# Kernel tuning notes

Hardware: AMD Instinct MI355X
Metric: run time of the kernel (lower is better)

## Reference

```python
import jax, jax.numpy as jnp
import numpy as np

# TT config: input_dimension=2048, output_multiplier=4, rank=16
# top_ranks    = [8,2,2,2,2,2,2,2,2]  (prod = 2048)
# bottom_ranks = [8,2,2,2,2,2,2,2,2]  (prod = 2048)
# core shapes (top, bottom, left, right): left/right are TT bond ranks.
CORE_SHAPES = [(8, 8, 1, 16)] + [(2, 2, 16, 16)] * 7 + [(2, 2, 16, 1)]


def setup_inputs() -> dict:
    key = jax.random.key(0)
    ks = jax.random.split(key, 10)
    inp = {"x": jax.random.normal(ks[0], (4, 2048, 2048), dtype=jnp.float32)}
    for i, s in enumerate(CORE_SHAPES):
        inp[f"p{i}"] = jax.random.normal(ks[i + 1], s, dtype=jnp.float32)
    return inp


def _tt_apply(x, ps):
    # x: [B, S, D] with D = prod(top_ranks) = 2048
    B, S, D = x.shape
    T = B * S
    # Normalize every core to (top, bottom, left_bond_in, right_bond_out).
    # Original einsum: '... abcdefghi, ajs, bkst, cltu, dmuv, envw, fowx, gpxy, hqzy, irz -> ... jklmnopqr'
    # Core 7 ('hqzy') has swapped bonds: its 4th dim (y) is the incoming bond
    # from core 6 and its 3rd dim (z) is the outgoing bond into core 8 ('irz').
    cores = list(ps[:7]) + [jnp.transpose(ps[7], (0, 1, 3, 2)), ps[8]]
    # core 0 is used as p0[:, :, 0, :] in the original; its left dim is 1 so
    # keeping the singleton left axis is identical math.
    y = x.reshape(T, 1, 1, D)  # [T, out_so_far=1, bond=1, remaining_top=D]
    J, M = 1, D
    for g in cores:
        tk, bk, lk, rk = g.shape
        y = y.reshape(T, J, lk, tk, M // tk)
        # contract incoming bond l and current top index a with the core
        y = jnp.einsum('tjlam,ablr->tjbrm', y, g)
        J *= bk
        M //= tk
        y = y.reshape(T, J, rk, M)
    # final: rk == 1, M == 1 -> [T, J] with J = prod(bottom_ranks) = 2048
    return y.reshape(B, S, J)


def reference(x, p0, p1, p2, p3, p4, p5, p6, p7, p8):
    return _tt_apply(x, (p0, p1, p2, p3, p4, p5, p6, p7, p8))
```

## Files before the change

kernel.cpp:

```cpp
#include <hip/hip_runtime.h>
#include <stdint.h>

typedef unsigned short u16;
typedef __bf16 bf16x8 __attribute__((ext_vector_type(8)));
typedef float f32x16 __attribute__((ext_vector_type(16)));
typedef u16 u16x8 __attribute__((ext_vector_type(8)));

__device__ __forceinline__ u16 f2bf(float f) {
  uint32_t u = __float_as_uint(f);
  u += 0x7fffu + ((u >> 16) & 1u);
  return (u16)(u >> 16);
}

__global__ __launch_bounds__(256) void build_lr_kernel(
    const float* __restrict__ p0, const float* __restrict__ p1,
    const float* __restrict__ p2, const float* __restrict__ p3,
    const float* __restrict__ p4, const float* __restrict__ p5,
    const float* __restrict__ p6, const float* __restrict__ p7,
    const float* __restrict__ p8, float* __restrict__ L4, float* __restrict__ R) {
  __shared__ float sC[5 * 1024];
  const int tid = threadIdx.x;
  if (blockIdx.x < 64) {
    for (int i = tid; i < 1024; i += 256) {
      sC[i]        = p0[i];
      sC[1024 + i] = p1[i];
      sC[2048 + i] = p2[i];
      sC[3072 + i] = p3[i];
      sC[4096 + i] = p4[i];
    }
    __syncthreads();
    const int idx = blockIdx.x * 256 + tid;
    const int AL = idx >> 7, BL = idx & 127;
    float t[16], u[16];
    const float* c0 = sC + ((AL >> 4) * 8 + (BL >> 4)) * 16;
#pragma unroll
    for (int l = 0; l < 16; l++) t[l] = c0[l];
#pragma unroll
    for (int k = 0; k < 4; k++) {
      const int ak = (AL >> (3 - k)) & 1;
      const int bk = (BL >> (3 - k)) & 1;
      const float* ck = sC + (k + 1) * 1024 + ((ak * 2 + bk) << 8);
#pragma unroll
      for (int r = 0; r < 16; r++) u[r] = 0.f;
#pragma unroll
      for (int l = 0; l < 16; l++) {
        const float tv = t[l];
#pragma unroll
        for (int r = 0; r < 16; r++) u[r] += tv * ck[l * 16 + r];
      }
#pragma unroll
      for (int r = 0; r < 16; r++) t[r] = u[r];
    }
    float4* dst = (float4*)(L4 + (size_t)idx * 16);
#pragma unroll
    for (int j = 0; j < 4; j++)
      dst[j] = make_float4(t[4 * j], t[4 * j + 1], t[4 * j + 2], t[4 * j + 3]);
  } else {
    for (int i = tid; i < 1024; i += 256) {
      sC[i]        = p5[i];
      sC[1024 + i] = p6[i];
      sC[2048 + i] = p7[i];
    }
    for (int i = tid; i < 64; i += 256) sC[3072 + i] = p8[i];
    __syncthreads();
    const int AR = tid >> 4, BR = tid & 15;
    const int a5 = AR >> 3, a6 = (AR >> 2) & 1, a7 = (AR >> 1) & 1, a8 = AR & 1;
    const int b5 = BR >> 3, b6 = (BR >> 2) & 1, b7 = (BR >> 1) & 1, b8 = BR & 1;
    float t[16], u[16];
    const float* c8 = sC + 3072 + (a8 * 2 + b8) * 16;
#pragma unroll
    for (int l = 0; l < 16; l++) t[l] = c8[l];
    const float* c7 = sC + 2048 + ((a7 * 2 + b7) << 8);
#pragma unroll
    for (int r = 0; r < 16; r++) u[r] = 0.f;
#pragma unroll
    for (int z = 0; z < 16; z++) {
      const float tv = t[z];
#pragma unroll
      for (int y = 0; y < 16; y++) u[y] += tv * c7[z * 16 + y];
    }
#pragma unroll
    for (int r = 0; r < 16; r++) t[r] = u[r];
    const float* c6 = sC + 1024 + ((a6 * 2 + b6) << 8);
#pragma unroll
    for (int rl = 0; rl < 16; rl++) {
      float s = 0.f;
#pragma unroll
      for (int rk = 0; rk < 16; rk++) s += t[rk] * c6[rl * 16 + rk];
      u[rl] = s;
    }
#pragma unroll
    for (int r = 0; r < 16; r++) t[r] = u[r];
    const float* c5 = sC + ((a5 * 2 + b5) << 8);
#pragma unroll
    for (int rl = 0; rl < 16; rl++) {
      float s = 0.f;
#pragma unroll
      for (int rk = 0; rk < 16; rk++) s += t[rk] * c5[rl * 16 + rk];
      R[tid * 16 + rl] = s;
    }
  }
}

__global__ __launch_bounds__(256) void prep_kernel(const float* __restrict__ L4,
                                                   const float* __restrict__ R,
                                                   u16* __restrict__ Wt,
                                                   const float* __restrict__ x,
                                                   u16* __restrict__ xb) {
  if (blockIdx.x < 2048) {
    int t = blockIdx.x * 256 + threadIdx.x;
    int e = t * 8;
    int Af = e & 2047;
    int Bf = e >> 11;
    const float* lrow = L4 + ((Af >> 4) * 128 + (Bf >> 4)) * 16;
    float lv[16];
#pragma unroll
    for (int r = 0; r < 16; r++) lv[r] = lrow[r];
    const float* rbase = R + (Bf & 15) * 16;
    u16x8 o;
#pragma unroll
    for (int j = 0; j < 8; j++) {
      const float* rrow = rbase + ((Af + j) & 15) * 256;
      float s = 0.f;
#pragma unroll
      for (int r = 0; r < 16; r++) s += lv[r] * rrow[r];
      o[j] = f2bf(s);
    }
    *(u16x8*)(Wt + (size_t)Bf * 2048 + Af) = o;
  } else {
    size_t i = ((size_t)(blockIdx.x - 2048) * 256 + threadIdx.x) * 8;
    float4 u = *(const float4*)(x + i);
    float4 v = *(const float4*)(x + i + 4);
    u16x8 o;
    o[0] = f2bf(u.x); o[1] = f2bf(u.y); o[2] = f2bf(u.z); o[3] = f2bf(u.w);
    o[4] = f2bf(v.x); o[5] = f2bf(v.y); o[6] = f2bf(v.z); o[7] = f2bf(v.w);
    *(u16x8*)(xb + i) = o;
  }
}

#define SB0() __builtin_amdgcn_sched_barrier(0)
#define LGKM(n) asm volatile("s_waitcnt lgkmcnt(" #n ")" ::: "memory")
#define VMCW(n) asm volatile("s_waitcnt vmcnt(" #n ")" ::: "memory")
#define BAR() asm volatile("s_barrier" ::: "memory")

#define STAGE1(Sbase, dsto, gp, uoff)                                          \
  __builtin_amdgcn_global_load_lds(                                            \
      (const __attribute__((address_space(1))) void*)((gp) + (uoff) + pl),     \
      (__attribute__((address_space(3))) void*)((Sbase) + (dsto) + ldst), 16, 0, 0)

#define STAGE_A(h, dsto, gk)                                                   \
  STAGE1(As, (dsto), A, uA + ((h)*128) * 2048 + (gk));                         \
  STAGE1(As, (dsto) + 4096, A, uA + ((h)*128 + 64) * 2048 + (gk))

#define STAGE_B(h, dsto, gk)                                                   \
  STAGE1(Bs, (dsto), B, uB + ((h)*128) * 2048 + (gk));                         \
  STAGE1(Bs, (dsto) + 4096, B, uB + ((h)*128 + 64) * 2048 + (gk))

#define LOAD_AF_H(dst, ah, m, pav)                                             \
  _Pragma("unroll") for (int ks = 0; ks < 4; ks++)                             \
      dst[ks] = *(const bf16x8*)(As + (pav) + (ah)*8192 + rbA + (m)*2048 +     \
                                 (((ks * 2 + hl) ^ key) * 8))

#define LOAD_BV(dst, bh, pav)                                                  \
  _Pragma("unroll") for (int ks = 0; ks < 4; ks++)                             \
      dst[ks] = *(const bf16x8*)(Bs + (pav) + (bh)*8192 + rbB +                \
                                 (((ks * 2 + hl) ^ key) * 8))

#define MFMA4(afh, bvv, accv)                                                  \
  _Pragma("unroll") for (int ks = 0; ks < 4; ks++)                             \
      accv = __builtin_amdgcn_mfma_f32_32x32x16_bf16(afh[ks], bvv[ks], accv, 0, 0, 0)

#define MFMA8I(afarr, bvv, accp)                                               \
  _Pragma("unroll") for (int ks = 0; ks < 4; ks++) {                           \
    accp[0] = __builtin_amdgcn_mfma_f32_32x32x16_bf16(afarr[0][ks], bvv[ks], accp[0], 0, 0, 0); \
    accp[1] = __builtin_amdgcn_mfma_f32_32x32x16_bf16(afarr[1][ks], bvv[ks], accp[1], 0, 0, 0); \
  }

__global__ __launch_bounds__(512, 2) void gemm_kernel(const u16* __restrict__ A,
                                                      const u16* __restrict__ B,
                                                      float* __restrict__ C) {
  __shared__ alignas(128) u16 As[4 * 8192];
  __shared__ alignas(128) u16 Bs[4 * 8192];
  const int tid = threadIdx.x;
  const int lane = tid & 63;
  const int w = tid >> 6;
  const int wr = w >> 2;
  const int wc = w & 3;
  const int r32 = lane & 31;
  const int hl = lane >> 5;

  const int F = blockIdx.x + (blockIdx.y << 3);
  const int li = F >> 3;
  const int m0 = ((F & 7) * 4 + (li >> 3)) << 8;
  const int n0 = (li & 7) << 8;

  const int srow = lane >> 3;
  const int soct = (lane & 7) ^ srow;
  const int uA = m0 * 2048;
  const int uB = n0 * 2048;
  const int pl = (w * 8 + srow) * 2048 + soct * 8;
  const int ldst = w * 512;

  const int key = r32 & 7;
  const int rbA = (wr * 64 + r32) * 64;
  const int rbB = (wc * 32 + r32) * 64;

  f32x16 acc[2][2][2] = {};
  bf16x8 af[2][4], bv0[4], bv1[4];

  STAGE_A(0, 0, 0);      SB0();
  STAGE_B(1, 8192, 0);   SB0();
  STAGE_A(1, 8192, 0);   SB0();
  STAGE_B(0, 0, 0);      SB0();
  STAGE_A(0, 16384, 64); SB0();
  STAGE_B(1, 24576, 64); SB0();
  STAGE_A(1, 24576, 64); SB0();
  VMCW(6);
  BAR();
  LOAD_BV(bv0, 0, 0);
  SB0();

#pragma unroll 1
  for (int t = 0; t < 32; t++) {
    const int pav = (t & 1) << 14;
    const int pnv = 16384 - pav;
    const int k1 = (t < 31 ? t + 1 : 31) * 64;
    const int k2 = (t < 30 ? t + 2 : 31) * 64;
    STAGE_B(0, pnv, k1);
    SB0();
    LOAD_AF_H(af[0], 0, 0, pav); SB0();
    LOAD_AF_H(af[1], 0, 1, pav); SB0();
    LOAD_BV(bv1, 1, pav);
    LGKM(8); SB0();
    __builtin_amdgcn_s_setprio(1);
    MFMA4(af[0], bv0, acc[0][0][0]);
    LGKM(4); SB0();
    MFMA4(af[1], bv0, acc[0][0][1]);
    __builtin_amdgcn_s_setprio(0);
    BAR();
    STAGE_A(0, pav, k2);
    LGKM(0); SB0();
    __builtin_amdgcn_s_setprio(1);
    MFMA8I(af, bv1, acc[0][1]);
    __builtin_amdgcn_s_setprio(0);
    BAR();
    STAGE_B(1, pav + 8192, k2);
    SB0();
    LOAD_AF_H(af[0], 1, 0, pav); SB0();
    LOAD_AF_H(af[1], 1, 1, pav);
    LGKM(4); SB0();
    __builtin_amdgcn_s_setprio(1);
    MFMA4(af[0], bv1, acc[1][1][0]);
    LGKM(0); SB0();
    MFMA4(af[1], bv1, acc[1][1][1]);
    __builtin_amdgcn_s_setprio(0);
    BAR();
    STAGE_A(1, pav + 8192, k2);
    SB0();
    __builtin_amdgcn_s_setprio(1);
    MFMA8I(af, bv0, acc[1][0]);
    __builtin_amdgcn_s_setprio(0);
    VMCW(6);
    BAR();
    LOAD_BV(bv0, 0, pnv);
    SB0();
  }

  VMCW(0);

#pragma unroll
  for (int ah = 0; ah < 2; ah++)
#pragma unroll
    for (int bh = 0; bh < 2; bh++)
#pragma unroll
      for (int m = 0; m < 2; m++) {
        size_t cbase = (size_t)(m0 + ah * 128 + wr * 64 + m * 32 + 4 * hl) * 2048 +
                       (n0 + bh * 128 + wc * 32 + r32);
#pragma unroll
        for (int reg = 0; reg < 16; reg++) {
          int row = (reg & 3) + 8 * (reg >> 2);
          __builtin_nontemporal_store(acc[ah][bh][m][reg], C + cbase + (size_t)row * 2048);
        }
      }
}

extern "C" void kernel_launch(void* const* d_in, const int* in_sizes, int n_in,
                              void* d_out, int out_size, void* d_ws, size_t ws_size,
                              hipStream_t stream) {
  const float* x = (const float*)d_in[0];
  const float* p0 = (const float*)d_in[1];
  const float* p1 = (const float*)d_in[2];
  const float* p2 = (const float*)d_in[3];
  const float* p3 = (const float*)d_in[4];
  const float* p4 = (const float*)d_in[5];
  const float* p5 = (const float*)d_in[6];
  const float* p6 = (const float*)d_in[7];
  const float* p7 = (const float*)d_in[8];
  const float* p8 = (const float*)d_in[9];
  char* ws = (char*)d_ws;
  u16* xbf = (u16*)ws;
  u16* Wt = (u16*)(ws + 33554432);
  float* L4 = (float*)(ws + 41943040);
  float* R = (float*)(ws + 42991616);

  build_lr_kernel<<<65, 256, 0, stream>>>(p0, p1, p2, p3, p4, p5, p6, p7, p8, L4, R);
  prep_kernel<<<10240, 256, 0, stream>>>(L4, R, Wt, x, xbf);
  gemm_kernel<<<dim3(8, 32), 512, 0, stream>>>(xbf, Wt, (float*)d_out);
}
```

Measured before the change: 224.7 us.

## Restructure GEMM main loop into k-slice register double-buffered pipeline

```diff
diff --git a/kernel.cpp b/kernel.cpp
--- a/kernel.cpp
+++ b/kernel.cpp
@@ -156,25 +156,24 @@
   STAGE1(Bs, (dsto), B, uB + ((h)*128) * 2048 + (gk));                         \
   STAGE1(Bs, (dsto) + 4096, B, uB + ((h)*128 + 64) * 2048 + (gk))
 
-#define LOAD_AF_H(dst, ah, m, pav)                                             \
-  _Pragma("unroll") for (int ks = 0; ks < 4; ks++)                             \
-      dst[ks] = *(const bf16x8*)(As + (pav) + (ah)*8192 + rbA + (m)*2048 +     \
-                                 (((ks * 2 + hl) ^ key) * 8))
-
-#define LOAD_BV(dst, bh, pav)                                                  \
-  _Pragma("unroll") for (int ks = 0; ks < 4; ks++)                             \
-      dst[ks] = *(const bf16x8*)(Bs + (pav) + (bh)*8192 + rbB +                \
-                                 (((ks * 2 + hl) ^ key) * 8))
-
-#define MFMA4(afh, bvv, accv)                                                  \
-  _Pragma("unroll") for (int ks = 0; ks < 4; ks++)                             \
-      accv = __builtin_amdgcn_mfma_f32_32x32x16_bf16(afh[ks], bvv[ks], accv, 0, 0, 0)
-
-#define MFMA8I(afarr, bvv, accp)                                               \
-  _Pragma("unroll") for (int ks = 0; ks < 4; ks++) {                           \
-    accp[0] = __builtin_amdgcn_mfma_f32_32x32x16_bf16(afarr[0][ks], bvv[ks], accp[0], 0, 0, 0); \
-    accp[1] = __builtin_amdgcn_mfma_f32_32x32x16_bf16(afarr[1][ks], bvv[ks], accp[1], 0, 0, 0); \
-  }
+#define READ_KS(aS, bS, ks, base)                                              \
+  _Pragma("unroll") for (int ah_ = 0; ah_ < 2; ah_++)                          \
+      _Pragma("unroll") for (int m_ = 0; m_ < 2; m_++)                         \
+          aS[ah_][m_] = *(const bf16x8*)(As + (base) + ah_ * 8192 + rbA +      \
+                                         m_ * 2048 + ((((ks)*2 + hl) ^ key) * 8)); \
+  _Pragma("unroll") for (int bh_ = 0; bh_ < 2; bh_++)                          \
+      bS[bh_] = *(const bf16x8*)(Bs + (base) + bh_ * 8192 + rbB +              \
+                                 ((((ks)*2 + hl) ^ key) * 8))
+
+#define MFMA_KS(aS, bS)                                                        \
+  acc[0][0][0] = __builtin_amdgcn_mfma_f32_32x32x16_bf16(aS[0][0], bS[0], acc[0][0][0], 0, 0, 0); \
+  acc[1][0][0] = __builtin_amdgcn_mfma_f32_32x32x16_bf16(aS[1][0], bS[0], acc[1][0][0], 0, 0, 0); \
+  acc[0][1][0] = __builtin_amdgcn_mfma_f32_32x32x16_bf16(aS[0][0], bS[1], acc[0][1][0], 0, 0, 0); \
+  acc[1][1][0] = __builtin_amdgcn_mfma_f32_32x32x16_bf16(aS[1][0], bS[1], acc[1][1][0], 0, 0, 0); \
+  acc[0][0][1] = __builtin_amdgcn_mfma_f32_32x32x16_bf16(aS[0][1], bS[0], acc[0][0][1], 0, 0, 0); \
+  acc[1][0][1] = __builtin_amdgcn_mfma_f32_32x32x16_bf16(aS[1][1], bS[0], acc[1][0][1], 0, 0, 0); \
+  acc[0][1][1] = __builtin_amdgcn_mfma_f32_32x32x16_bf16(aS[0][1], bS[1], acc[0][1][1], 0, 0, 0); \
+  acc[1][1][1] = __builtin_amdgcn_mfma_f32_32x32x16_bf16(aS[1][1], bS[1], acc[1][1][1], 0, 0, 0)
 
 __global__ __launch_bounds__(512, 2) void gemm_kernel(const u16* __restrict__ A,
                                                       const u16* __restrict__ B,
@@ -206,18 +205,15 @@
   const int rbB = (wc * 32 + r32) * 64;
 
   f32x16 acc[2][2][2] = {};
-  bf16x8 af[2][4], bv0[4], bv1[4];
-
-  STAGE_A(0, 0, 0);      SB0();
-  STAGE_B(1, 8192, 0);   SB0();
-  STAGE_A(1, 8192, 0);   SB0();
-  STAGE_B(0, 0, 0);      SB0();
-  STAGE_A(0, 16384, 64); SB0();
-  STAGE_B(1, 24576, 64); SB0();
-  STAGE_A(1, 24576, 64); SB0();
-  VMCW(6);
+  bf16x8 a0_[2][2], b0_[2];
+  bf16x8 a1_[2][2], b1_[2];
+
+  STAGE_A(0, 0, 0); STAGE_A(1, 8192, 0);
+  STAGE_B(0, 0, 0); STAGE_B(1, 8192, 0);
+  VMCW(0);
   BAR();
-  LOAD_BV(bv0, 0, 0);
+  SB0();
+  READ_KS(a0_, b0_, 0, 0);
   SB0();
 
 #pragma unroll 1
@@ -225,47 +221,45 @@
     const int pav = (t & 1) << 14;
     const int pnv = 16384 - pav;
     const int k1 = (t < 31 ? t + 1 : 31) * 64;
-    const int k2 = (t < 30 ? t + 2 : 31) * 64;
-    STAGE_B(0, pnv, k1);
-    SB0();
-    LOAD_AF_H(af[0], 0, 0, pav); SB0();
-    LOAD_AF_H(af[1], 0, 1, pav); SB0();
-    LOAD_BV(bv1, 1, pav);
-    LGKM(8); SB0();
+    STAGE_A(0, pnv, k1); STAGE_A(1, pnv + 8192, k1);
+    STAGE_B(0, pnv, k1); STAGE_B(1, pnv + 8192, k1);
+    SB0();
+    READ_KS(a1_, b1_, 1, pav);
+    SB0();
+    LGKM(6); SB0();
     __builtin_amdgcn_s_setprio(1);
-    MFMA4(af[0], bv0, acc[0][0][0]);
-    LGKM(4); SB0();
-    MFMA4(af[1], bv0, acc[0][0][1]);
+    MFMA_KS(a0_, b0_);
     __builtin_amdgcn_s_setprio(0);
+    SB0();
+    READ_KS(a0_, b0_, 2, pav);
+    SB0();
+    LGKM(6); SB0();
+    __builtin_amdgcn_s_setprio(1);
+    MFMA_KS(a1_, b1_);
+    __builtin_amdgcn_s_setprio(0);
+    SB0();
+    READ_KS(a1_, b1_, 3, pav);
+    SB0();
+    LGKM(6); SB0();
+    __builtin_amdgcn_s_setprio(1);
+    MFMA_KS(a0_, b0_);
+    __builtin_amdgcn_s_setprio(0);
+    SB0();
+    VMCW(0);
     BAR();
-    STAGE_A(0, pav, k2);
-    LGKM(0); SB0();
+    SB0();
+    READ_KS(a0_, b0_, 0, pnv);
+    SB0();
+    LGKM(6); SB0();
     __builtin_amdgcn_s_setprio(1);
-    MFMA8I(af, bv1, acc[0][1]);
+    MFMA_KS(a1_, b1_);
     __builtin_amdgcn_s_setprio(0);
+    SB0();
     BAR();
-    STAGE_B(1, pav + 8192, k2);
-    SB0();
-    LOAD_AF_H(af[0], 1, 0, pav); SB0();
-    LOAD_AF_H(af[1], 1, 1, pav);
-    LGKM(4); SB0();
-    __builtin_amdgcn_s_setprio(1);
-    MFMA4(af[0], bv1, acc[1][1][0]);
-    LGKM(0); SB0();
-    MFMA4(af[1], bv1, acc[1][1][1]);
-    __builtin_amdgcn_s_setprio(0);
-    BAR();
-    STAGE_A(1, pav + 8192, k2);
-    SB0();
-    __builtin_amdgcn_s_setprio(1);
-    MFMA8I(af, bv0, acc[1][0]);
-    __builtin_amdgcn_s_setprio(0);
-    VMCW(6);
-    BAR();
-    LOAD_BV(bv0, 0, pnv);
     SB0();
   }
 
+  LGKM(0);
   VMCW(0);
 
 #pragma unroll
```

Result: faster. 220.2 us (-2.0%).
